# Kernel tuning notes

Hardware: AMD Instinct MI355X
Metric: run time of the kernel (lower is better)

## Reference

```python
import jax, jax.numpy as jnp
import numpy as np

N = 50000
E = 1_600_000
IN_F = 128
OUT_F = 128
EMB = 3
KER = 4


def setup_inputs() -> dict:
    key = jax.random.key(0)
    k1, k2, k3, k4, k5 = jax.random.split(key, 5)
    x = jax.random.normal(k1, (N, IN_F), dtype=jnp.float32)
    edge_idx = jax.random.randint(k2, (2, E), 0, N, dtype=jnp.int64)
    # learned parameters (init mirrors reset_parameters, except sig=1.0 so
    # the Gaussian edge weights are non-degenerate)
    weight = 0.1 * jax.random.normal(k3, (IN_F, OUT_F, KER), dtype=jnp.float32)
    bias = 0.1 * jax.random.normal(k4, (OUT_F,), dtype=jnp.float32)
    mu = 0.005 * jax.random.normal(k5, (EMB, KER), dtype=jnp.float32)
    sig = jnp.ones((1, KER), dtype=jnp.float32)
    return {"x": x, "edge_idx": edge_idx, "weight": weight, "bias": bias, "mu": mu, "sig": sig}


def reference(x, edge_idx, weight, bias, mu, sig):
    n = x.shape[0]
    ker = weight.shape[2]
    row, col = edge_idx[0], edge_idx[1]
    domain = x[:, :3]                      # [N, 3]
    diff = domain[row] - domain[col]       # [E, 3]
    out = jnp.zeros((n, weight.shape[1]), dtype=x.dtype)
    for k in range(ker):                   # small fixed kernel loop (as in source)
        support = x @ weight[:, :, k]      # [N, out]
        # Gaussian edge weight: exp(sig_k * (-0.5 * ||diff - mu_k||^2))
        value = jnp.exp(sig[0, k] * (-0.5 * jnp.sum((diff - mu[:, k]) ** 2, axis=1)))  # [E]
        # sparse.mm(A, support): out[row] += value * support[col]
        msgs = value[:, None] * support[col]              # [E, out]
        out = out + jax.ops.segment_sum(msgs, row, num_segments=n)
    return out + bias
```

## Files before the change

kernel.cpp:

```cpp
#include <hip/hip_runtime.h>

#define IN_F 128
#define OUT_F 128
#define KER 4
#define SLOT 80

typedef unsigned int uint;
typedef unsigned short u16;
typedef __attribute__((ext_vector_type(8))) short bf16x8;
typedef __attribute__((ext_vector_type(4))) float f32x4;
typedef __attribute__((ext_vector_type(2))) float f32x2;

__device__ __forceinline__ uint f2bf(float f) {
    uint u = __float_as_uint(f);
    u += 0x7fffu + ((u >> 16) & 1u);
    return u >> 16;
}


__global__ void __launch_bounds__(256) prep_kernel(
    const float* __restrict__ x, const float* __restrict__ weight,
    const float* __restrict__ mu, const float* __restrict__ sig,
    const int* __restrict__ row, const int* __restrict__ col, int n, int E,
    u16* __restrict__ xbf, float4* __restrict__ dom, u16* __restrict__ W2p,
    u16* __restrict__ ru16, u16* __restrict__ cu16,
    float* __restrict__ kc, int* __restrict__ cursor,
    int nB1, int nB2, int nBE) {
    const int b = blockIdx.x;
    if (b < nB1) {
        int t = b * 256 + threadIdx.x;
        if (t < n * 32) {
            float4 v = *reinterpret_cast<const float4*>(x + (size_t)t * 4);
            uint2 o;
            o.x = f2bf(v.x) | (f2bf(v.y) << 16);
            o.y = f2bf(v.z) | (f2bf(v.w) << 16);
            *reinterpret_cast<uint2*>(xbf + (size_t)t * 4) = o;
            if ((t & 31) == 0) dom[t >> 5] = make_float4(v.x, v.y, v.z, 0.f);
        }
    } else if (b < nB1 + nB2) {
        int t = (b - nB1) * 256 + threadIdx.x;
        if (t < 8192) {
            int lane = t & 63;
            int nfks = t >> 6;
            int ks = nfks & 15, nf = nfks >> 4;
            int f = nf * 16 + (lane & 15);
            int kbase = ks * 32 + ((lane >> 4) << 3);
            uint pk[4];
            #pragma unroll
            for (int jj = 0; jj < 4; ++jj) {
                int k0 = kbase + jj * 2;
                int c0 = k0 & 127, q0 = k0 >> 7;
                int k1 = k0 + 1;
                int c1 = k1 & 127, q1 = k1 >> 7;
                uint lo = f2bf(weight[((size_t)c0 * OUT_F + f) * KER + q0]);
                uint hi = f2bf(weight[((size_t)c1 * OUT_F + f) * KER + q1]);
                pk[jj] = lo | (hi << 16);
            }
            *reinterpret_cast<uint4*>(W2p + (size_t)t * 8) =
                make_uint4(pk[0], pk[1], pk[2], pk[3]);
        }
    } else if (b < nB1 + nB2 + nBE) {
        int t = (b - nB1 - nB2) * 256 + threadIdx.x;
        int e0 = t * 4;
        if (e0 + 3 < E) {
            int4 rv = *reinterpret_cast<const int4*>(row + e0);
            int4 cv = *reinterpret_cast<const int4*>(col + e0);
            ushort4 ro, co;
            ro.x = (u16)rv.x; ro.y = (u16)rv.y; ro.z = (u16)rv.z; ro.w = (u16)rv.w;
            co.x = (u16)cv.x; co.y = (u16)cv.y; co.z = (u16)cv.z; co.w = (u16)cv.w;
            *reinterpret_cast<ushort4*>(ru16 + e0) = ro;
            *reinterpret_cast<ushort4*>(cu16 + e0) = co;
        } else {
            for (int e = e0; e < E; ++e) { ru16[e] = (u16)row[e]; cu16[e] = (u16)col[e]; }
        }
    } else {
        int rgn = b - nB1 - nB2 - nBE;
        int t = rgn * 256 + threadIdx.x;
        if (t < n) cursor[t] = 0;
        if (rgn == 0 && threadIdx.x < KER) {
            int k = threadIdx.x;
            float sg = sig[k];
            float m0 = mu[k], m1 = mu[KER + k], m2 = mu[2 * KER + k];
            kc[k * 5 + 0] = -0.5f * sg * (m0 * m0 + m1 * m1 + m2 * m2);
            kc[k * 5 + 1] = -0.5f * sg;
            kc[k * 5 + 2] = sg * m0;
            kc[k * 5 + 3] = sg * m1;
            kc[k * 5 + 4] = sg * m2;
        }
    }
}

__global__ void __launch_bounds__(256) place_kernel(
    const u16* __restrict__ ru16, const u16* __restrict__ cu16, int E, int n, int NB,
    int* __restrict__ cursor, const float4* __restrict__ dom,
    const float* __restrict__ kc, uint4* __restrict__ recs) {
    const int b = blockIdx.x, x = b & 7, g = b >> 3;
    const int wp = (n + 7) >> 3;
    const int r_lo = x * wp;
    const int r_hi = min(n, r_lo + wp);
    const int S = (E + NB - 1) / NB;
    const int base = g * S;
    const int lim = min(base + S, E);
    float A[4], B[4], C0[4], C1[4], C2[4];
    #pragma unroll
    for (int k = 0; k < 4; ++k) {
        A[k]  = kc[k * 5 + 0];
        B[k]  = kc[k * 5 + 1];
        C0[k] = kc[k * 5 + 2];
        C1[k] = kc[k * 5 + 3];
        C2[k] = kc[k * 5 + 4];
    }
    for (int e0 = base + threadIdx.x; e0 < lim; e0 += 1024) {
        int rr[4], cc[4];
        bool act[4];
        #pragma unroll
        for (int u = 0; u < 4; ++u) {
            int e = e0 + u * 256;
            bool inb = e < lim;
            rr[u] = inb ? (int)ru16[e] : 0;
            act[u] = inb && (rr[u] >= r_lo) && (rr[u] < r_hi);
            cc[u] = act[u] ? (int)cu16[e] : 0;
        }
        float4 drv[4], dcv[4];
        #pragma unroll
        for (int u = 0; u < 4; ++u)
            if (act[u]) { drv[u] = dom[rr[u]]; dcv[u] = dom[cc[u]]; }
        #pragma unroll
        for (int u = 0; u < 4; ++u) {
            if (!act[u]) continue;
            float d0 = drv[u].x - dcv[u].x, d1 = drv[u].y - dcv[u].y, d2 = drv[u].z - dcv[u].z;
            float Sq = fmaf(d2, d2, fmaf(d1, d1, d0 * d0));
            uint vb[4];
            #pragma unroll
            for (int k = 0; k < 4; ++k) {
                float t = fmaf(B[k], Sq, A[k]);
                t = fmaf(C0[k], d0, t);
                t = fmaf(C1[k], d1, t);
                t = fmaf(C2[k], d2, t);
                vb[k] = f2bf(__expf(t));
            }
            int rank = atomicAdd(&cursor[rr[u]], 1);
            if (rank < SLOT) {
                int pos = rr[u] * SLOT + rank;
                recs[pos] = make_uint4(vb[0] | (vb[1] << 16), vb[2] | (vb[3] << 16),
                                       (uint)cc[u], 0u);
            }
        }
    }
}


__global__ void __launch_bounds__(256) agg_kernel(
    const u16* __restrict__ xbf, const int* __restrict__ cursor,
    const uint4* __restrict__ recs, u16* __restrict__ aggbf, int n) {
    const int w = threadIdx.x >> 6, l = threadIdx.x & 63;
    const int i = blockIdx.x * 4 + w;
    if (i >= n) return;
    const int start = i * SLOT;
    const int end   = start + min(cursor[i], SLOT);

    f32x2 acc[4];
    #pragma unroll
    for (int k = 0; k < 4; ++k) acc[k] = (f32x2){0.f, 0.f};

    auto body = [&](uint lo, uint hi, uint xp) {
        f32x2 xv;
        xv.x = __uint_as_float(xp << 16);
        xv.y = __uint_as_float(xp & 0xffff0000u);
        float v0 = __uint_as_float(lo << 16);
        float v1 = __uint_as_float(lo & 0xffff0000u);
        float v2 = __uint_as_float(hi << 16);
        float v3 = __uint_as_float(hi & 0xffff0000u);
        acc[0] += v0 * xv;
        acc[1] += v1 * xv;
        acc[2] += v2 * xv;
        acc[3] += v3 * xv;
    };

    const u16* xl = xbf + (l << 1);
    int j = start;
    for (; j + 8 <= end; j += 8) {
        uint4 rc[8];
        uint xp[8];
        #pragma unroll
        for (int u = 0; u < 8; ++u) rc[u] = recs[j + u];
        #pragma unroll
        for (int u = 0; u < 8; ++u)
            xp[u] = *reinterpret_cast<const uint*>(xl + ((size_t)rc[u].z << 7));
        #pragma unroll
        for (int u = 0; u < 8; ++u) body(rc[u].x, rc[u].y, xp[u]);
    }
    for (; j < end; ++j) {
        uint4 rc = recs[j];
        uint xp = *reinterpret_cast<const uint*>(xl + ((size_t)rc.z << 7));
        body(rc.x, rc.y, xp);
    }

    u16* o = aggbf + ((size_t)i << 9) + (l << 1);
    *reinterpret_cast<uint*>(o +   0) = f2bf(acc[0].x) | (f2bf(acc[0].y) << 16);
    *reinterpret_cast<uint*>(o + 128) = f2bf(acc[1].x) | (f2bf(acc[1].y) << 16);
    *reinterpret_cast<uint*>(o + 256) = f2bf(acc[2].x) | (f2bf(acc[2].y) << 16);
    *reinterpret_cast<uint*>(o + 384) = f2bf(acc[3].x) | (f2bf(acc[3].y) << 16);
}


__global__ void __launch_bounds__(256) gemm_kernel(
    const u16* __restrict__ aggbf, const u16* __restrict__ W2p,
    const float* __restrict__ bias, float* __restrict__ out, int n) {
    const int w = threadIdx.x >> 6, l = threadIdx.x & 63;
    const int r0 = blockIdx.x * 128 + w * 32;
    int ra = r0 + (l & 15);
    int rb = ra + 16;
    if (ra > n - 1) ra = n - 1;
    if (rb > n - 1) rb = n - 1;
    const u16* pa = aggbf + ((size_t)ra << 9) + ((l >> 4) << 3);
    const u16* pb = aggbf + ((size_t)rb << 9) + ((l >> 4) << 3);
    const u16* wp = W2p + ((size_t)l << 3);

    f32x4 acc[2][8];
    #pragma unroll
    for (int m = 0; m < 2; ++m)
        #pragma unroll
        for (int nf = 0; nf < 8; ++nf)
            acc[m][nf] = (f32x4){0.f, 0.f, 0.f, 0.f};

    #pragma unroll 2
    for (int ks = 0; ks < 16; ++ks) {
        bf16x8 a0 = *reinterpret_cast<const bf16x8*>(pa + ks * 32);
        bf16x8 a1 = *reinterpret_cast<const bf16x8*>(pb + ks * 32);
        #pragma unroll
        for (int nf = 0; nf < 8; ++nf) {
            bf16x8 bfr = *reinterpret_cast<const bf16x8*>(wp + (((nf << 4) + ks) << 9));
            acc[0][nf] = __builtin_amdgcn_mfma_f32_16x16x32_bf16(a0, bfr, acc[0][nf], 0, 0, 0);
            acc[1][nf] = __builtin_amdgcn_mfma_f32_16x16x32_bf16(a1, bfr, acc[1][nf], 0, 0, 0);
        }
    }

    const int cq = l >> 4;
    const int cr = l & 15;
    #pragma unroll
    for (int nf = 0; nf < 8; ++nf) {
        float bv = bias[(nf << 4) + cr];
        #pragma unroll
        for (int m = 0; m < 2; ++m) {
            #pragma unroll
            for (int rg = 0; rg < 4; ++rg) {
                int rowi = r0 + m * 16 + cq * 4 + rg;
                if (rowi < n)
                    out[(size_t)rowi * OUT_F + (nf << 4) + cr] = acc[m][nf][rg] + bv;
            }
        }
    }
}


extern "C" void kernel_launch(void* const* d_in, const int* in_sizes, int n_in,
                              void* d_out, int out_size, void* d_ws, size_t ws_size,
                              hipStream_t stream) {
    const float* x      = (const float*)d_in[0];
    const int*   edge   = (const int*)d_in[1];
    const float* weight = (const float*)d_in[2];
    const float* bias   = (const float*)d_in[3];
    const float* mu     = (const float*)d_in[4];
    const float* sig    = (const float*)d_in[5];
    float* out = (float*)d_out;

    const int n = in_sizes[0] / IN_F;
    const int E = in_sizes[1] / 2;
    const int* row = edge;
    const int* col = edge + E;

    char* ws = (char*)d_ws;
    size_t off = 0;
    auto alloc = [&](size_t bytes) {
        size_t o = off;
        off = (off + bytes + 255) & ~(size_t)255;
        return o;
    };
    u16*    xbf      = (u16*)(ws + alloc((size_t)n * IN_F * 2));
    float4* dom      = (float4*)(ws + alloc((size_t)n * 16));
    uint4*  recs     = (uint4*)(ws + alloc((size_t)n * SLOT * 16));
    u16*    aggbf    = (u16*)(ws + alloc((size_t)n * KER * IN_F * 2));
    u16*    W2p      = (u16*)(ws + alloc((size_t)KER * IN_F * OUT_F * 2));
    u16*    ru16     = (u16*)(ws + alloc((size_t)E * 2));
    u16*    cu16     = (u16*)(ws + alloc((size_t)E * 2));
    int*    cursor   = (int*)(ws + alloc((size_t)n * 4));
    float*  kc       = (float*)(ws + alloc(32 * 4));
    if (off > ws_size) return;

    const int nB1 = (n * 32 + 255) / 256;
    const int nB2 = 32;
    const int nBE = ((E + 3) / 4 + 255) / 256;
    const int nB4 = (n + 255) / 256;
    prep_kernel<<<nB1 + nB2 + nBE + nB4, 256, 0, stream>>>(
        x, weight, mu, sig, row, col, n, E, xbf, dom, W2p, ru16, cu16,
        kc, cursor, nB1, nB2, nBE);

    const int NB = 512;
    place_kernel<<<NB * 8, 256, 0, stream>>>(ru16, cu16, E, n, NB, cursor, dom, kc, recs);
    agg_kernel<<<(n + 3) / 4, 256, 0, stream>>>(xbf, cursor, recs, aggbf, n);
    gemm_kernel<<<(n + 127) / 128, 256, 0, stream>>>(aggbf, W2p, bias, out, n);
}
```

Baseline: 273.6 us.

## Split edge records into packed value and u16 column arrays; XCD-aware agg mapping

Replaces the 16-byte per-edge record (4 bf16 weights, column, padding) with a separate 8-byte value array and a 2-byte column array. This cuts the record footprint from 16 to 10 bytes per edge and lets the aggregation kernel fetch eight columns in one 16-byte load. The agg kernel also remaps blocks so that blockIdx&7 selects a row range, matching the place kernel's partitioning. The likely intent is to keep rows on the same XCD's L2 that wrote them. The cost is two extra scattered writes per edge in placement, and the vectorised uint4 load of colp assumes 16-byte alignment (SLOT=80 keeps this true).

```diff
diff --git a/kernel.cpp b/kernel.cpp
--- a/kernel.cpp
+++ b/kernel.cpp
@@ -93,7 +93,7 @@
 __global__ void __launch_bounds__(256) place_kernel(
     const u16* __restrict__ ru16, const u16* __restrict__ cu16, int E, int n, int NB,
     int* __restrict__ cursor, const float4* __restrict__ dom,
-    const float* __restrict__ kc, uint4* __restrict__ recs) {
+    const float* __restrict__ kc, uint* __restrict__ vals, u16* __restrict__ colp) {
     const int b = blockIdx.x, x = b & 7, g = b >> 3;
     const int wp = (n + 7) >> 3;
     const int r_lo = x * wp;
@@ -142,8 +142,9 @@
             int rank = atomicAdd(&cursor[rr[u]], 1);
             if (rank < SLOT) {
                 int pos = rr[u] * SLOT + rank;
-                recs[pos] = make_uint4(vb[0] | (vb[1] << 16), vb[2] | (vb[3] << 16),
-                                       (uint)cc[u], 0u);
+                *reinterpret_cast<uint2*>(vals + (size_t)pos * 2) =
+                    make_uint2(vb[0] | (vb[1] << 16), vb[2] | (vb[3] << 16));
+                colp[pos] = (u16)cc[u];
             }
         }
     }
@@ -152,10 +153,14 @@
 
 __global__ void __launch_bounds__(256) agg_kernel(
     const u16* __restrict__ xbf, const int* __restrict__ cursor,
-    const uint4* __restrict__ recs, u16* __restrict__ aggbf, int n) {
+    const uint* __restrict__ vals, const u16* __restrict__ colp,
+    u16* __restrict__ aggbf, int n) {
     const int w = threadIdx.x >> 6, l = threadIdx.x & 63;
-    const int i = blockIdx.x * 4 + w;
-    if (i >= n) return;
+    const int x = blockIdx.x & 7, q = blockIdx.x >> 3;
+    const int wp = (n + 7) >> 3;
+    const int i = x * wp + q * 4 + w;
+    const int r_hi = min(n, x * wp + wp);
+    if (i >= r_hi) return;
     const int start = i * SLOT;
     const int end   = start + min(cursor[i], SLOT);
 
@@ -178,22 +183,40 @@
     };
 
     const u16* xl = xbf + (l << 1);
+    const uint4* v4 = reinterpret_cast<const uint4*>(vals);
     int j = start;
     for (; j + 8 <= end; j += 8) {
-        uint4 rc[8];
-        uint xp[8];
-        #pragma unroll
-        for (int u = 0; u < 8; ++u) rc[u] = recs[j + u];
-        #pragma unroll
-        for (int u = 0; u < 8; ++u)
-            xp[u] = *reinterpret_cast<const uint*>(xl + ((size_t)rc[u].z << 7));
-        #pragma unroll
-        for (int u = 0; u < 8; ++u) body(rc[u].x, rc[u].y, xp[u]);
+        uint4 cw = *reinterpret_cast<const uint4*>(colp + j);
+        uint4 p0 = v4[(j >> 1) + 0];
+        uint4 p1 = v4[(j >> 1) + 1];
+        uint4 p2 = v4[(j >> 1) + 2];
+        uint4 p3 = v4[(j >> 1) + 3];
+        uint c0 = cw.x & 0xffffu, c1 = cw.x >> 16;
+        uint c2 = cw.y & 0xffffu, c3 = cw.y >> 16;
+        uint c4 = cw.z & 0xffffu, c5 = cw.z >> 16;
+        uint c6 = cw.w & 0xffffu, c7 = cw.w >> 16;
+        uint xp0 = *reinterpret_cast<const uint*>(xl + ((size_t)c0 << 7));
+        uint xp1 = *reinterpret_cast<const uint*>(xl + ((size_t)c1 << 7));
+        uint xp2 = *reinterpret_cast<const uint*>(xl + ((size_t)c2 << 7));
+        uint xp3 = *reinterpret_cast<const uint*>(xl + ((size_t)c3 << 7));
+        uint xp4 = *reinterpret_cast<const uint*>(xl + ((size_t)c4 << 7));
+        uint xp5 = *reinterpret_cast<const uint*>(xl + ((size_t)c5 << 7));
+        uint xp6 = *reinterpret_cast<const uint*>(xl + ((size_t)c6 << 7));
+        uint xp7 = *reinterpret_cast<const uint*>(xl + ((size_t)c7 << 7));
+        body(p0.x, p0.y, xp0);
+        body(p0.z, p0.w, xp1);
+        body(p1.x, p1.y, xp2);
+        body(p1.z, p1.w, xp3);
+        body(p2.x, p2.y, xp4);
+        body(p2.z, p2.w, xp5);
+        body(p3.x, p3.y, xp6);
+        body(p3.z, p3.w, xp7);
     }
     for (; j < end; ++j) {
-        uint4 rc = recs[j];
-        uint xp = *reinterpret_cast<const uint*>(xl + ((size_t)rc.z << 7));
-        body(rc.x, rc.y, xp);
+        uint2 pv = *reinterpret_cast<const uint2*>(vals + (size_t)j * 2);
+        uint c = colp[j];
+        uint xp = *reinterpret_cast<const uint*>(xl + ((size_t)c << 7));
+        body(pv.x, pv.y, xp);
     }
 
     u16* o = aggbf + ((size_t)i << 9) + (l << 1);
@@ -279,7 +302,8 @@
     };
     u16*    xbf      = (u16*)(ws + alloc((size_t)n * IN_F * 2));
     float4* dom      = (float4*)(ws + alloc((size_t)n * 16));
-    uint4*  recs     = (uint4*)(ws + alloc((size_t)n * SLOT * 16));
+    uint*   vals     = (uint*)(ws + alloc((size_t)n * SLOT * 8));
+    u16*    colp     = (u16*)(ws + alloc((size_t)n * SLOT * 2));
     u16*    aggbf    = (u16*)(ws + alloc((size_t)n * KER * IN_F * 2));
     u16*    W2p      = (u16*)(ws + alloc((size_t)KER * IN_F * OUT_F * 2));
     u16*    ru16     = (u16*)(ws + alloc((size_t)E * 2));
@@ -297,7 +321,10 @@
         kc, cursor, nB1, nB2, nBE);
 
     const int NB = 512;
-    place_kernel<<<NB * 8, 256, 0, stream>>>(ru16, cu16, E, n, NB, cursor, dom, kc, recs);
-    agg_kernel<<<(n + 3) / 4, 256, 0, stream>>>(xbf, cursor, recs, aggbf, n);
+    place_kernel<<<NB * 8, 256, 0, stream>>>(ru16, cu16, E, n, NB, cursor, dom, kc,
+                                             vals, colp);
+    const int wp = (n + 7) >> 3;
+    const int perslot = (wp + 3) / 4;
+    agg_kernel<<<perslot * 8, 256, 0, stream>>>(xbf, cursor, vals, colp, aggbf, n);
     gemm_kernel<<<(n + 127) / 128, 256, 0, stream>>>(aggbf, W2p, bias, out, n);
 }
```

Result: slower. 280.8 us (+2.6%).
